# Optimization experiments

Measured on AMD Instinct MI355X. Metric: run time of the kernel, lower is better.

The kernel has to match this reference:

```python
import jax, jax.numpy as jnp
import numpy as np

S, B, H = 2048, 2, 2048
NH = 16
HD = H // NH  # 128
ROPE_BASE = 10000.0


def _rope_cos_sin(seq_len, dim, dtype):
    inv_freq = 1.0 / (ROPE_BASE ** (jnp.arange(0, dim, 2, dtype=jnp.float32) / dim))
    t = jnp.arange(seq_len, dtype=jnp.float32)
    freqs = jnp.outer(t, inv_freq)            # [S, dim/2]
    emb = jnp.concatenate([freqs, freqs], -1)  # [S, dim]
    return jnp.cos(emb).astype(dtype), jnp.sin(emb).astype(dtype)


def _rotate_half(x):
    x1, x2 = jnp.split(x, 2, axis=-1)
    return jnp.concatenate([-x2, x1], axis=-1)


def setup_inputs() -> dict:
    key = jax.random.key(0)
    k1, k2, k3 = jax.random.split(key, 3)
    hidden_states = jax.random.normal(k1, (S, B, H), dtype=jnp.float32)
    w_qkv = jax.random.normal(k2, (3 * H, H), dtype=jnp.float32) * (1.0 / np.sqrt(H))
    w_out = jax.random.normal(k3, (H, H), dtype=jnp.float32) * (1.0 / np.sqrt(H))
    return {"hidden_states": hidden_states, "w_qkv": w_qkv, "w_out": w_out}


def reference(hidden_states, w_qkv, w_out):
    seq_len, batch, _ = hidden_states.shape
    # QKV projection (nn.Linear: x @ W^T), bias=False
    qkv = jnp.einsum('sbh,oh->sbo', hidden_states, w_qkv)
    qkv = qkv.reshape(seq_len, batch, 3, NH, HD)
    q, k, v = qkv[:, :, 0], qkv[:, :, 1], qkv[:, :, 2]  # [S, B, NH, HD]

    cos, sin = _rope_cos_sin(seq_len, HD, hidden_states.dtype)
    cos = cos[:, None, None, :]
    sin = sin[:, None, None, :]
    q = q * cos + _rotate_half(q) * sin
    k = k * cos + _rotate_half(k) * sin

    # [S, B, NH, HD] -> [B, NH, S, HD]
    q = q.transpose(1, 2, 0, 3)
    k = k.transpose(1, 2, 0, 3)
    v = v.transpose(1, 2, 0, 3)

    scale = 1.0 / np.sqrt(HD)
    scores = jnp.einsum('bhqd,bhkd->bhqk', q, k) * scale
    causal = jnp.tril(jnp.ones((seq_len, seq_len), dtype=bool))
    scores = jnp.where(causal, scores, jnp.finfo(scores.dtype).min)
    probs = jax.nn.softmax(scores, axis=-1)
    attn = jnp.einsum('bhqk,bhkd->bhqd', probs, v)  # [B, NH, S, HD]

    # [B, NH, S, HD] -> [S, B, NH*HD]
    out = attn.transpose(2, 0, 1, 3).reshape(seq_len, batch, -1)
    out = jnp.einsum('sbh,oh->sbo', out, w_out)
    return out
```

## Files before the change

kernel.cpp:

```cpp
#include <hip/hip_runtime.h>
#include <hip/hip_bf16.h>

typedef __attribute__((ext_vector_type(8))) short bf16x8;
typedef __attribute__((ext_vector_type(8))) short s16x8;
typedef __attribute__((ext_vector_type(4))) float f32x4;
typedef __attribute__((ext_vector_type(4))) int i32x4;

#define SEQ 2048
#define BATCH 2
#define HID 2048
#define NH 16
#define HD 128
#define QKVN 6144

static __device__ __forceinline__ short f2bf(float f) {
    union { float f; unsigned u; } v; v.f = f;
    unsigned r = (v.u + 0x7FFFu + ((v.u >> 16) & 1u)) >> 16;
    return (short)r;
}

static __device__ __forceinline__ void gload_lds16(const short* g, short* l) {
    __builtin_amdgcn_global_load_lds((const __attribute__((address_space(1))) void*)g,
                                     (__attribute__((address_space(3))) void*)l, 16, 0, 0);
}

__global__ void cvt_kernel(const float* __restrict__ in, short* __restrict__ out, int n8) {
    const int i = blockIdx.x * 256 + threadIdx.x;
    if (i >= n8) return;
    f32x4 a = *(const f32x4*)(in + (size_t)i * 8);
    f32x4 b = *(const f32x4*)(in + (size_t)i * 8 + 4);
    s16x8 o = { f2bf(a.x), f2bf(a.y), f2bf(a.z), f2bf(a.w),
                f2bf(b.x), f2bf(b.y), f2bf(b.z), f2bf(b.w) };
    *(s16x8*)(out + (size_t)i * 8) = o;
}

#define STAGE_A(BUF, H, KK) do { \
    const short* _s = aSrc + (size_t)(H) * 64 * K + (KK) * 64; \
    short* _d = lds + (BUF) * 16384 + (H) * 8192 + w * 512; \
    gload_lds16(_s, _d); \
    gload_lds16(_s + (size_t)128 * K, _d + 4096); \
} while (0)

#define STAGE_B(BUF, H, KK) do { \
    const short* _s = bSrc + (size_t)(H) * 32 * K + (KK) * 64; \
    short* _d = lds + 32768 + (BUF) * 16384 + (H) * 8192 + w * 512; \
    gload_lds16(_s, _d); \
    gload_lds16(_s + (size_t)128 * K, _d + 4096); \
} while (0)

#define LOAD_A(MH) do { \
    const short* _p = lds + bufR * 16384 + (MH) * 8192 + aOff0; \
    const short* _q = lds + bufR * 16384 + (MH) * 8192 + aOff1; \
    _Pragma("unroll") \
    for (int mm = 0; mm < 4; ++mm) { \
        aR[mm][0] = *(const bf16x8*)(_p + mm * 1024); \
        aR[mm][1] = *(const bf16x8*)(_q + mm * 1024); \
    } \
} while (0)

#define LOAD_B(NHh) do { \
    const short* _p = lds + 32768 + bufR * 16384 + (NHh) * 8192 + bOff0; \
    const short* _q = lds + 32768 + bufR * 16384 + (NHh) * 8192 + bOff1; \
    _Pragma("unroll") \
    for (int nn = 0; nn < 2; ++nn) { \
        bR[(NHh) * 2 + nn][0] = *(const bf16x8*)(_p + nn * 1024); \
        bR[(NHh) * 2 + nn][1] = *(const bf16x8*)(_q + nn * 1024); \
    } \
} while (0)

#define MFMA_Q(MH, NHh) do { \
    _Pragma("unroll") \
    for (int mm = 0; mm < 4; ++mm) { \
        _Pragma("unroll") \
        for (int nn = 0; nn < 2; ++nn) { \
            f32x4 _c = acc[(MH) * 4 + mm][(NHh) * 2 + nn]; \
            _c = __builtin_amdgcn_mfma_f32_16x16x32_bf16(aR[mm][0], bR[(NHh) * 2 + nn][0], _c, 0, 0, 0); \
            _c = __builtin_amdgcn_mfma_f32_16x16x32_bf16(aR[mm][1], bR[(NHh) * 2 + nn][1], _c, 0, 0, 0); \
            acc[(MH) * 4 + mm][(NHh) * 2 + nn] = _c; \
        } \
    } \
} while (0)

__global__ __launch_bounds__(512, 2)
void gemm256(const short* __restrict__ A, const short* __restrict__ B,
             short* __restrict__ C, int N, int K) {
    __shared__ short lds[65536];

    const int tid = threadIdx.x;
    const int mBase = blockIdx.y * 256;
    const int nBase = blockIdx.x * 256;
    const int w = tid >> 6, lane = tid & 63, quad = lane >> 4, l15 = lane & 15;
    const int wm = w >> 2, wn = w & 3;

    const int kcol = 8 * ((tid & 7) ^ ((tid >> 3) & 7));
    const short* aSrc = A + (size_t)(mBase + (tid >> 3)) * K + kcol;
    const short* bSrc = B + (size_t)(nBase + ((tid >> 3) & 31) + ((tid >> 8) & 1) * 64) * K + kcol;

    const int cs0 = (quad * 8) ^ ((l15 & 7) << 3);
    const int aOff0 = (l15 + wm * 64) * 64 + cs0;
    const int aOff1 = aOff0 ^ 32;
    const int bOff0 = (l15 + wn * 32) * 64 + cs0;
    const int bOff1 = bOff0 ^ 32;

    const int NK = K >> 6;
    f32x4 acc[8][4] = {};
    bf16x8 aR[4][2], bR[4][2];

    STAGE_A(0, 0, 0); STAGE_B(0, 0, 0); STAGE_B(0, 1, 0); STAGE_A(0, 1, 0);
    STAGE_A(1, 0, 1); STAGE_B(1, 0, 1); STAGE_B(1, 1, 1);
    asm volatile("s_waitcnt vmcnt(6)" ::: "memory");
    __builtin_amdgcn_s_barrier();

    int bufR = 0;
    for (int k = 0; k < NK; ++k) {
        const int kk1 = (k + 1 < NK) ? k + 1 : NK - 1;
        const int kk2 = (k + 2 < NK) ? k + 2 : NK - 1;
        LOAD_A(0);
        LOAD_B(0);
        STAGE_A(bufR ^ 1, 1, kk1);
        asm volatile("s_waitcnt lgkmcnt(8)" ::: "memory");
        __builtin_amdgcn_s_barrier();
        asm volatile("s_waitcnt lgkmcnt(0)" ::: "memory");
        __builtin_amdgcn_s_setprio(1);
        MFMA_Q(0, 0);
        __builtin_amdgcn_s_setprio(0);
        __builtin_amdgcn_s_barrier();
        LOAD_B(1);
        STAGE_A(bufR, 0, kk2);
        __builtin_amdgcn_s_barrier();
        asm volatile("s_waitcnt lgkmcnt(0)" ::: "memory");
        __builtin_amdgcn_s_setprio(1);
        MFMA_Q(0, 1);
        __builtin_amdgcn_s_setprio(0);
        __builtin_amdgcn_s_barrier();
        LOAD_A(1);
        STAGE_B(bufR, 0, kk2);
        __builtin_amdgcn_s_barrier();
        asm volatile("s_waitcnt lgkmcnt(0)" ::: "memory");
        __builtin_amdgcn_s_setprio(1);
        MFMA_Q(1, 1);
        __builtin_amdgcn_s_setprio(0);
        __builtin_amdgcn_s_barrier();
        STAGE_B(bufR, 1, kk2);
        asm volatile("s_waitcnt vmcnt(6)" ::: "memory");
        __builtin_amdgcn_s_barrier();
        __builtin_amdgcn_s_setprio(1);
        MFMA_Q(1, 0);
        __builtin_amdgcn_s_setprio(0);
        __builtin_amdgcn_s_barrier();
        bufR ^= 1;
    }
    asm volatile("s_waitcnt vmcnt(0)" ::: "memory");

    #pragma unroll
    for (int f = 0; f < 8; ++f) {
        const int row0 = mBase + wm * 128 + f * 16 + quad * 4;
        #pragma unroll
        for (int g = 0; g < 4; ++g) {
            const int col = nBase + wn * 64 + g * 16 + l15;
            #pragma unroll
            for (int r = 0; r < 4; ++r)
                C[(size_t)(row0 + r) * N + col] = f2bf(acc[f][g][r]);
        }
    }
}

template<bool STORE_BF16>
__global__ __launch_bounds__(256, 2)
void gemm_bt(const short* __restrict__ A, const short* __restrict__ B,
             void* __restrict__ Cp, int N, int K) {
    __shared__ short As[128 * 32];
    __shared__ short Bs[128 * 32];

    const int tid = threadIdx.x;
    const int mBase = blockIdx.y * 128;
    const int nBase = blockIdx.x * 128;
    const int w = tid >> 6, lane = tid & 63, quad = lane >> 4, l15 = lane & 15;
    const int wr = (w >> 1) * 64, wc = (w & 1) * 64;

    const int r0 = tid >> 2;
    const int kc = (tid & 3) * 8;
    const short* aG = A + (size_t)(mBase + r0) * K + kc;
    const short* bG = B + (size_t)(nBase + r0) * K + kc;
    short* ldsA0 = As + w * 512;
    short* ldsA1 = As + 2048 + w * 512;
    short* ldsB0 = Bs + w * 512;
    short* ldsB1 = Bs + 2048 + w * 512;

    f32x4 acc[4][4] = {};

    for (int k0 = 0; k0 < K; k0 += 32) {
        __syncthreads();
        gload_lds16(aG + k0,                    ldsA0);
        gload_lds16(aG + (size_t)64 * K + k0,   ldsA1);
        gload_lds16(bG + k0,                    ldsB0);
        gload_lds16(bG + (size_t)64 * K + k0,   ldsB1);
        __syncthreads();

        bf16x8 af[4], bfb[4];
        #pragma unroll
        for (int i = 0; i < 4; ++i)
            af[i] = *(const bf16x8*)(As + (wr + i * 16 + l15) * 32 + quad * 8);
        #pragma unroll
        for (int j = 0; j < 4; ++j)
            bfb[j] = *(const bf16x8*)(Bs + (wc + j * 16 + l15) * 32 + quad * 8);
        #pragma unroll
        for (int i = 0; i < 4; ++i)
            #pragma unroll
            for (int j = 0; j < 4; ++j)
                acc[i][j] = __builtin_amdgcn_mfma_f32_16x16x32_bf16(af[i], bfb[j], acc[i][j], 0, 0, 0);
    }

    #pragma unroll
    for (int i = 0; i < 4; ++i) {
        const int row0 = mBase + wr + i * 16 + quad * 4;
        #pragma unroll
        for (int j = 0; j < 4; ++j) {
            const int col = nBase + wc + j * 16 + l15;
            #pragma unroll
            for (int r = 0; r < 4; ++r) {
                if (STORE_BF16)
                    ((short*)Cp)[(size_t)(row0 + r) * N + col] = f2bf(acc[i][j][r]);
                else
                    ((float*)Cp)[(size_t)(row0 + r) * N + col] = acc[i][j][r];
            }
        }
    }
}

__global__ void rope_kernel(short* __restrict__ qkv) {
    const int tid = blockIdx.x * 256 + threadIdx.x;
    const int d     = tid & 63;
    const int h     = (tid >> 6) & 15;
    const int which = (tid >> 10) & 1;
    const int b     = (tid >> 11) & 1;
    const int s     = tid >> 12;

    const size_t base = (size_t)(s * 2 + b) * QKVN + which * 2048 + h * 128;
    const float inv_freq = expf(-((float)(2 * d) * (1.0f / 128.0f)) * 9.210340371976184f);
    float sn, cs;
    sincosf((float)s * inv_freq, &sn, &cs);
    const float post = (which == 0) ? 0.08838834764831845f : 1.0f;

    union { unsigned u; float f; } x1, x2;
    x1.u = ((unsigned)(unsigned short)qkv[base + d]) << 16;
    x2.u = ((unsigned)(unsigned short)qkv[base + d + 64]) << 16;
    qkv[base + d]      = f2bf((x1.f * cs - x2.f * sn) * post);
    qkv[base + d + 64] = f2bf((x2.f * cs + x1.f * sn) * post);
}

__global__ void vtrans_kernel(const short* __restrict__ qkv, short* __restrict__ vT) {
    __shared__ short T[64][72];
    const int s0 = blockIdx.x * 64, d0 = blockIdx.y * 64;
    const int bh = blockIdx.z;
    const int b = bh >> 4, h = bh & 15;
    const int t = threadIdx.x;

    #pragma unroll
    for (int p = 0; p < 2; ++p) {
        const int sl = (t >> 3) + p * 32;
        const int dl = (t & 7) * 8;
        *(i32x4*)&T[sl][dl] =
            *(const i32x4*)(qkv + (size_t)((s0 + sl) * 2 + b) * QKVN + 4096 + h * 128 + d0 + dl);
    }
    __syncthreads();
    #pragma unroll
    for (int p = 0; p < 2; ++p) {
        const int dl = (t >> 3) + p * 32;
        const int sl = (t & 7) * 8;
        short tmp[8];
        #pragma unroll
        for (int j = 0; j < 8; ++j) tmp[j] = T[sl + j][dl];
        *(i32x4*)(vT + ((size_t)bh * 128 + d0 + dl) * 2048 + s0 + sl) = *(i32x4*)tmp;
    }
}

__global__ __launch_bounds__(256, 2)
void attn_kernel(const short* __restrict__ qkv, const short* __restrict__ vT,
                 short* __restrict__ out) {
    __shared__ short lds[40960];

    const int bx = blockIdx.x;
    const int h = blockIdx.y, b = blockIdx.z;
    const int Aq = (bx & 1) ? (bx >> 1) : (15 - (bx >> 1));
    const int qt = b ? (15 - Aq) : Aq;
    const int tid = threadIdx.x;
    const int w = tid >> 6, lane = tid & 63, quad = lane >> 4, l15 = lane & 15;
    const int bh = b * 16 + h;
    const int cswz = (l15 & 7) << 3;

    bf16x8 aq[2][4];
    #pragma unroll
    for (int m = 0; m < 2; ++m) {
        const short* qbase =
            qkv + (size_t)((qt * 128 + w * 32 + m * 16 + l15) * 2 + b) * QKVN + h * 128;
        #pragma unroll
        for (int c = 0; c < 4; ++c)
            aq[m][c] = *(const bf16x8*)(qbase + c * 32 + quad * 8);
    }

    f32x4 oacc[2][8] = {};
    float lpart[2][4] = {};

    const short* kSrc0 = qkv + (size_t)((w * 16 + (lane >> 4)) * 2 + b) * QKVN
                       + 2048 + h * 128 + ((lane & 15) ^ (lane >> 4)) * 8;
    const short* kSrc1 = qkv + (size_t)((w * 16 + 4 + (lane >> 4)) * 2 + b) * QKVN
                       + 2048 + h * 128 + ((lane & 15) ^ (4 | (lane >> 4))) * 8;
    const short* vSrc = vT + ((size_t)bh * 128 + w * 32 + (lane >> 3)) * 2048
                      + ((lane & 7) ^ ((lane >> 3) & 7)) * 8;
    short* kDst = lds + w * 2048;
    short* vDst = lds + 16384 + w * 2048;

#define STAGE_KV(BUF, KK0) do { \
    const size_t kAdv = (size_t)(KK0) * 2 * QKVN; \
    short* _kd = kDst + (BUF) * 8192; \
    short* _vd = vDst + (BUF) * 8192; \
    gload_lds16(kSrc0 + kAdv,                  _kd); \
    gload_lds16(kSrc1 + kAdv,                  _kd + 512); \
    gload_lds16(kSrc0 + kAdv + 16 * QKVN,      _kd + 1024); \
    gload_lds16(kSrc1 + kAdv + 16 * QKVN,      _kd + 1536); \
    gload_lds16(vSrc + (KK0),                  _vd); \
    gload_lds16(vSrc + (KK0) + 8 * 2048,       _vd + 512); \
    gload_lds16(vSrc + (KK0) + 16 * 2048,      _vd + 1024); \
    gload_lds16(vSrc + (KK0) + 24 * 2048,      _vd + 1536); \
} while (0)

    const int nChunks = 2 * qt + 2;

    STAGE_KV(0, 0);
    asm volatile("s_waitcnt vmcnt(0)" ::: "memory");
    __builtin_amdgcn_s_barrier();

    for (int ck = 0; ck < nChunks; ++ck) {
        const int cur = ck & 1;
        const int kk0 = ck * 64;
        if (ck + 1 < nChunks) STAGE_KV(cur ^ 1, kk0 + 64);

        const short* Kc = lds + cur * 8192;
        const short* Vc = lds + 16384 + cur * 8192;
        short* Pw = lds + 32768 + w * 2048;

        f32x4 sc4[2][4] = {};
        #pragma unroll
        for (int c = 0; c < 4; ++c) {
            const int cb = (c * 32 + quad * 8) ^ cswz;
            #pragma unroll
            for (int n = 0; n < 4; ++n) {
                bf16x8 bk = *(const bf16x8*)(Kc + (n * 16 + l15) * 128 + cb);
                sc4[0][n] = __builtin_amdgcn_mfma_f32_16x16x32_bf16(aq[0][c], bk, sc4[0][n], 0, 0, 0);
                sc4[1][n] = __builtin_amdgcn_mfma_f32_16x16x32_bf16(aq[1][c], bk, sc4[1][n], 0, 0, 0);
            }
        }

        const bool diag = (ck >= 2 * qt);
        #pragma unroll
        for (int m = 0; m < 2; ++m) {
            const int rowbase = qt * 128 + w * 32 + m * 16 + quad * 4;
            #pragma unroll
            for (int r = 0; r < 4; ++r) {
                const int prow = m * 16 + quad * 4 + r;
                const int pswz = ((quad * 4 + r) & 7) << 3;
                #pragma unroll
                for (int n = 0; n < 4; ++n) {
                    float sv = sc4[m][n][r];
                    if (diag && (kk0 + n * 16 + l15 > rowbase + r)) sv = -1e30f;
                    const float p = __expf(sv);
                    lpart[m][r] += p;
                    Pw[prow * 64 + ((n * 16 + l15) ^ pswz)] = f2bf(p);
                }
            }
        }

        #pragma unroll
        for (int kp2 = 0; kp2 < 2; ++kp2) {
            const int cb = (kp2 * 32 + quad * 8) ^ cswz;
            bf16x8 ap0 = *(const bf16x8*)(Pw + l15 * 64 + cb);
            bf16x8 ap1 = *(const bf16x8*)(Pw + (16 + l15) * 64 + cb);
            #pragma unroll
            for (int dt = 0; dt < 8; ++dt) {
                bf16x8 bv = *(const bf16x8*)(Vc + (dt * 16 + l15) * 64 + cb);
                oacc[0][dt] = __builtin_amdgcn_mfma_f32_16x16x32_bf16(ap0, bv, oacc[0][dt], 0, 0, 0);
                oacc[1][dt] = __builtin_amdgcn_mfma_f32_16x16x32_bf16(ap1, bv, oacc[1][dt], 0, 0, 0);
            }
        }

        asm volatile("s_waitcnt vmcnt(0)" ::: "memory");
        __builtin_amdgcn_s_barrier();
    }
#undef STAGE_KV

    #pragma unroll
    for (int m = 0; m < 2; ++m) {
        const int rowbase = qt * 128 + w * 32 + m * 16 + quad * 4;
        #pragma unroll
        for (int r = 0; r < 4; ++r) {
            float l = lpart[m][r];
            #pragma unroll
            for (int off = 1; off < 16; off <<= 1)
                l += __shfl_xor(l, off);
            const float inv_l = 1.0f / l;
            const size_t obase = (size_t)((rowbase + r) * 2 + b) * HID + h * 128;
            #pragma unroll
            for (int dt = 0; dt < 8; ++dt)
                out[obase + dt * 16 + l15] = f2bf(oacc[m][dt][r] * inv_l);
        }
    }
}

extern "C" void kernel_launch(void* const* d_in, const int* in_sizes, int n_in,
                              void* d_out, int out_size, void* d_ws, size_t ws_size,
                              hipStream_t stream) {
    const float* hidden = (const float*)d_in[0];
    const float* w_qkv  = (const float*)d_in[1];
    const float* w_out  = (const float*)d_in[2];
    float* out = (float*)d_out;

    short* qkv     = (short*)d_ws;
    short* attnb   = qkv + (size_t)4096 * QKVN;
    short* wqkv_bf = attnb + (size_t)4096 * HID;
    short* wout_bf = wqkv_bf;
    short* hbf     = wqkv_bf + (size_t)QKVN * HID;
    short* vT      = hbf;

    dim3 blk(256);
    cvt_kernel<<<dim3(4096), blk, 0, stream>>>(hidden, hbf, 4096 * 256);
    cvt_kernel<<<dim3(6144), blk, 0, stream>>>(w_qkv, wqkv_bf, 6144 * 256);
    gemm256<<<dim3(QKVN / 256, 4096 / 256), dim3(512), 0, stream>>>(
        hbf, wqkv_bf, qkv, QKVN, HID);
    cvt_kernel<<<dim3(2048), blk, 0, stream>>>(w_out, wout_bf, 2048 * 256);
    rope_kernel<<<dim3((SEQ * BATCH * 2 * NH * (HD / 2)) / 256), blk, 0, stream>>>(qkv);
    vtrans_kernel<<<dim3(SEQ / 64, HD / 64, BATCH * NH), blk, 0, stream>>>(qkv, vT);
    attn_kernel<<<dim3(SEQ / 128, NH, BATCH), blk, 0, stream>>>(qkv, vT, attnb);
    gemm_bt<false><<<dim3(HID / 128, 4096 / 128), blk, 0, stream>>>(
        attnb, wout_bf, out, HID, HID);
}
```

Baseline: 387.4 us.

## Replace output-projection GEMM with 256x128 pipelined, swizzled 512-thread kernel

```diff
diff --git a/kernel.cpp b/kernel.cpp
--- a/kernel.cpp
+++ b/kernel.cpp
@@ -165,65 +165,135 @@
     }
 }
 
-template<bool STORE_BF16>
-__global__ __launch_bounds__(256, 2)
-void gemm_bt(const short* __restrict__ A, const short* __restrict__ B,
-             void* __restrict__ Cp, int N, int K) {
-    __shared__ short As[128 * 32];
-    __shared__ short Bs[128 * 32];
+#define G128_STAGE_A(BUF, HA, KK) do { \
+    const short* _s = ((HA) ? aS1 : aS0) + (size_t)(KK) * 64; \
+    short* _d = lds + (BUF) * 16384 + (HA) * 8192 + w * 512; \
+    gload_lds16(_s, _d); \
+    gload_lds16(_s + (size_t)128 * K, _d + 4096); \
+} while (0)
+
+#define G128_STAGE_B(BUF, HB, KK) do { \
+    const short* _s = ((HB) ? bS1 : bS0) + (size_t)(KK) * 64; \
+    short* _d = lds + 32768 + (BUF) * 8192 + (HB) * 4096 + w * 512; \
+    gload_lds16(_s, _d); \
+} while (0)
+
+#define G128_LOAD_A(HA) do { \
+    const short* _p = lds + bufR * 16384 + (HA) * 8192; \
+    _Pragma("unroll") \
+    for (int mm = 0; mm < 2; ++mm) { \
+        aR[mm][0] = *(const bf16x8*)(_p + aOff0 + mm * 1024); \
+        aR[mm][1] = *(const bf16x8*)(_p + aOff1 + mm * 1024); \
+    } \
+} while (0)
+
+#define G128_LOAD_B(HB) do { \
+    const short* _p = lds + 32768 + bufR * 8192 + (HB) * 4096; \
+    _Pragma("unroll") \
+    for (int nn = 0; nn < 2; ++nn) { \
+        bR[(HB) * 2 + nn][0] = *(const bf16x8*)(_p + bOff0 + nn * 1024); \
+        bR[(HB) * 2 + nn][1] = *(const bf16x8*)(_p + bOff1 + nn * 1024); \
+    } \
+} while (0)
+
+#define G128_MFMA(HA, HB) do { \
+    _Pragma("unroll") \
+    for (int mm = 0; mm < 2; ++mm) { \
+        _Pragma("unroll") \
+        for (int nn = 0; nn < 2; ++nn) { \
+            f32x4 _c = acc[(HA) * 2 + mm][(HB) * 2 + nn]; \
+            _c = __builtin_amdgcn_mfma_f32_16x16x32_bf16(aR[mm][0], bR[(HB) * 2 + nn][0], _c, 0, 0, 0); \
+            _c = __builtin_amdgcn_mfma_f32_16x16x32_bf16(aR[mm][1], bR[(HB) * 2 + nn][1], _c, 0, 0, 0); \
+            acc[(HA) * 2 + mm][(HB) * 2 + nn] = _c; \
+        } \
+    } \
+} while (0)
+
+__global__ __launch_bounds__(512, 2)
+void gemm128n(const short* __restrict__ A, const short* __restrict__ B,
+              float* __restrict__ C, int N, int K) {
+    __shared__ short lds[49152];
 
     const int tid = threadIdx.x;
-    const int mBase = blockIdx.y * 128;
+    const int mBase = blockIdx.y * 256;
     const int nBase = blockIdx.x * 128;
     const int w = tid >> 6, lane = tid & 63, quad = lane >> 4, l15 = lane & 15;
-    const int wr = (w >> 1) * 64, wc = (w & 1) * 64;
-
-    const int r0 = tid >> 2;
-    const int kc = (tid & 3) * 8;
-    const short* aG = A + (size_t)(mBase + r0) * K + kc;
-    const short* bG = B + (size_t)(nBase + r0) * K + kc;
-    short* ldsA0 = As + w * 512;
-    short* ldsA1 = As + 2048 + w * 512;
-    short* ldsB0 = Bs + w * 512;
-    short* ldsB1 = Bs + 2048 + w * 512;
-
+    const int wm = w >> 1, wn = w & 1;
+
+    const int kcol = 8 * ((tid & 7) ^ ((tid >> 3) & 7));
+    const int srow = ((tid >> 3) & 15) + (tid >> 7) * 32;
+    const short* aS0 = A + (size_t)(mBase + srow) * K + kcol;
+    const short* aS1 = aS0 + (size_t)16 * K;
+    const short* bS0 = B + (size_t)(nBase + srow) * K + kcol;
+    const short* bS1 = bS0 + (size_t)16 * K;
+
+    const int cs0 = (quad * 8) ^ ((l15 & 7) << 3);
+    const int aOff0 = (l15 + wm * 32) * 64 + cs0;
+    const int aOff1 = aOff0 ^ 32;
+    const int bOff0 = (l15 + wn * 32) * 64 + cs0;
+    const int bOff1 = bOff0 ^ 32;
+
+    const int NK = K >> 6;
     f32x4 acc[4][4] = {};
-
-    for (int k0 = 0; k0 < K; k0 += 32) {
-        __syncthreads();
-        gload_lds16(aG + k0,                    ldsA0);
-        gload_lds16(aG + (size_t)64 * K + k0,   ldsA1);
-        gload_lds16(bG + k0,                    ldsB0);
-        gload_lds16(bG + (size_t)64 * K + k0,   ldsB1);
-        __syncthreads();
-
-        bf16x8 af[4], bfb[4];
-        #pragma unroll
-        for (int i = 0; i < 4; ++i)
-            af[i] = *(const bf16x8*)(As + (wr + i * 16 + l15) * 32 + quad * 8);
-        #pragma unroll
-        for (int j = 0; j < 4; ++j)
-            bfb[j] = *(const bf16x8*)(Bs + (wc + j * 16 + l15) * 32 + quad * 8);
-        #pragma unroll
-        for (int i = 0; i < 4; ++i)
-            #pragma unroll
-            for (int j = 0; j < 4; ++j)
-                acc[i][j] = __builtin_amdgcn_mfma_f32_16x16x32_bf16(af[i], bfb[j], acc[i][j], 0, 0, 0);
-    }
+    bf16x8 aR[2][2], bR[4][2];
+
+    G128_STAGE_A(0, 0, 0); G128_STAGE_B(0, 0, 0); G128_STAGE_B(0, 1, 0); G128_STAGE_A(0, 1, 0);
+    G128_STAGE_A(1, 0, 1); G128_STAGE_B(1, 0, 1); G128_STAGE_B(1, 1, 1);
+    asm volatile("s_waitcnt vmcnt(4)" ::: "memory");
+    __builtin_amdgcn_s_barrier();
+
+    int bufR = 0;
+    for (int k = 0; k < NK; ++k) {
+        const int kk1 = (k + 1 < NK) ? k + 1 : NK - 1;
+        const int kk2 = (k + 2 < NK) ? k + 2 : NK - 1;
+        G128_LOAD_A(0);
+        G128_LOAD_B(0);
+        G128_STAGE_A(bufR ^ 1, 1, kk1);
+        asm volatile("s_waitcnt lgkmcnt(4)" ::: "memory");
+        __builtin_amdgcn_s_barrier();
+        asm volatile("s_waitcnt lgkmcnt(0)" ::: "memory");
+        __builtin_amdgcn_s_setprio(1);
+        G128_MFMA(0, 0);
+        __builtin_amdgcn_s_setprio(0);
+        __builtin_amdgcn_s_barrier();
+        G128_LOAD_B(1);
+        G128_STAGE_A(bufR, 0, kk2);
+        __builtin_amdgcn_s_barrier();
+        asm volatile("s_waitcnt lgkmcnt(0)" ::: "memory");
+        __builtin_amdgcn_s_setprio(1);
+        G128_MFMA(0, 1);
+        __builtin_amdgcn_s_setprio(0);
+        __builtin_amdgcn_s_barrier();
+        G128_LOAD_A(1);
+        G128_STAGE_B(bufR, 0, kk2);
+        __builtin_amdgcn_s_barrier();
+        asm volatile("s_waitcnt lgkmcnt(0)" ::: "memory");
+        __builtin_amdgcn_s_setprio(1);
+        G128_MFMA(1, 1);
+        __builtin_amdgcn_s_setprio(0);
+        __builtin_amdgcn_s_barrier();
+        G128_STAGE_B(bufR, 1, kk2);
+        asm volatile("s_waitcnt vmcnt(4)" ::: "memory");
+        __builtin_amdgcn_s_barrier();
+        __builtin_amdgcn_s_setprio(1);
+        G128_MFMA(1, 0);
+        __builtin_amdgcn_s_setprio(0);
+        __builtin_amdgcn_s_barrier();
+        bufR ^= 1;
+    }
+    asm volatile("s_waitcnt vmcnt(0)" ::: "memory");
 
     #pragma unroll
-    for (int i = 0; i < 4; ++i) {
-        const int row0 = mBase + wr + i * 16 + quad * 4;
-        #pragma unroll
-        for (int j = 0; j < 4; ++j) {
-            const int col = nBase + wc + j * 16 + l15;
-            #pragma unroll
-            for (int r = 0; r < 4; ++r) {
-                if (STORE_BF16)
-                    ((short*)Cp)[(size_t)(row0 + r) * N + col] = f2bf(acc[i][j][r]);
-                else
-                    ((float*)Cp)[(size_t)(row0 + r) * N + col] = acc[i][j][r];
-            }
+    for (int af = 0; af < 4; ++af) {
+        const int ha = af >> 1, mm = af & 1;
+        const int row0 = mBase + wm * 64 + (2 * mm + ha) * 16 + quad * 4;
+        #pragma unroll
+        for (int bg = 0; bg < 4; ++bg) {
+            const int hb = bg >> 1, nn = bg & 1;
+            const int col = nBase + wn * 64 + (2 * nn + hb) * 16 + l15;
+            #pragma unroll
+            for (int r = 0; r < 4; ++r)
+                C[(size_t)(row0 + r) * N + col] = acc[af][bg][r];
         }
     }
 }
@@ -431,6 +501,6 @@
     rope_kernel<<<dim3((SEQ * BATCH * 2 * NH * (HD / 2)) / 256), blk, 0, stream>>>(qkv);
     vtrans_kernel<<<dim3(SEQ / 64, HD / 64, BATCH * NH), blk, 0, stream>>>(qkv, vT);
     attn_kernel<<<dim3(SEQ / 128, NH, BATCH), blk, 0, stream>>>(qkv, vT, attnb);
-    gemm_bt<false><<<dim3(HID / 128, 4096 / 128), blk, 0, stream>>>(
+    gemm128n<<<dim3(HID / 128, 4096 / 256), dim3(512), 0, stream>>>(
         attnb, wout_bf, out, HID, HID);
 }
```

Result: faster. 377.9 us (-2.5%).
